# Optimization experiments

Measured on AMD Instinct MI355X. Metric: run time of the kernel, lower is better.

The kernel has to match this reference:

```python
import jax, jax.numpy as jnp
import numpy as np

DMODEL = 512
NUM_HEADS = 8
HEAD_DIM = DMODEL // NUM_HEADS
ATTN_LEN = 5
BATCH = 4
SEQ = 4096


def kv_roll(t, layer, shift):
    # t: [B, h_sub, T, 1, hd]; replicates tf.pad + tf.roll + concat + slice
    T = t.shape[2]
    dil = 2 ** layer
    p = dil * (ATTN_LEN // 2)
    tp = jnp.pad(t, ((0, 0), (0, 0), (p, p), (0, 0), (0, 0)))
    # circular rolls, concat along the singleton window axis -> [B,h,T+2p,ATTN_LEN,hd]
    rolled = jnp.concatenate(
        [jnp.roll(tp, -i * dil, axis=2) for i in range(shift, ATTN_LEN + shift)],
        axis=3,
    )
    return rolled[:, :, :T]


def setup_inputs() -> dict:
    key = jax.random.key(0)
    ks = jax.random.split(key, 8)
    inputs = jax.random.normal(ks[0], (BATCH, SEQ, DMODEL), dtype=jnp.float32)
    Wq = jax.random.normal(ks[1], (DMODEL, DMODEL), dtype=jnp.float32) * 0.02
    bq = jnp.zeros((DMODEL,), dtype=jnp.float32)
    Wk = jax.random.normal(ks[2], (DMODEL, DMODEL), dtype=jnp.float32) * 0.02
    bk = jnp.zeros((DMODEL,), dtype=jnp.float32)
    Wv = jax.random.normal(ks[3], (DMODEL, DMODEL), dtype=jnp.float32) * 0.02
    bv = jnp.zeros((DMODEL,), dtype=jnp.float32)
    Er = jax.random.normal(ks[4], (NUM_HEADS, HEAD_DIM, ATTN_LEN), dtype=jnp.float32) * 0.05
    return {"inputs": inputs, "Wq": Wq, "bq": bq, "Wk": Wk, "bk": bk,
            "Wv": Wv, "bv": bv, "Er": Er, "layer": 1}


def reference(inputs, Wq, bq, Wk, bk, Wv, bv, Er, layer):
    B, T, D = inputs.shape
    # projections -> [B, H, T, 1, hd]
    def proj(W, b):
        x = inputs @ W + b
        x = x.reshape(B, T, NUM_HEADS, 1, HEAD_DIM)
        return jnp.transpose(x, (0, 2, 1, 3, 4))
    q = proj(Wq, bq)
    k = proj(Wk, bk)
    v = proj(Wv, bv)

    def build_windows(t):
        # per-head-group shifts: heads 0-3 shift 0, head 4 shift -2, head 5 -1, head 6 +1, head 7 +2
        return jnp.concatenate((
            kv_roll(t[:, 0:4], layer, 0),
            kv_roll(t[:, 4:5], layer, -2),
            kv_roll(t[:, 5:6], layer, -1),
            kv_roll(t[:, 6:7], layer, 1),
            kv_roll(t[:, 7:8], layer, 2),
        ), axis=1)  # [B, H, T, ATTN_LEN, hd]

    kw = build_windows(k)
    vw = build_windows(v)

    # qk: [B, H, T, 1, ATTN_LEN]
    qk = jnp.einsum('bhtqd,bhtwd->bhtqw', q, kw)
    # relative positional bias: q @ Er -> [B, H, T, 1, ATTN_LEN]
    qEr = jnp.einsum('bhtqd,hdw->bhtqw', q, Er)
    scale = jnp.sqrt(jnp.float32(HEAD_DIM)).astype(inputs.dtype)
    logits = (qk + qEr) / scale
    mask = (qk == 0).astype(logits.dtype)
    attn = jax.nn.softmax(logits + mask * -10000.0, axis=-1)
    # out: [B, H, T, 1, hd]
    out = jnp.einsum('bhtqw,bhtwd->bhtqd', attn, vw)
    out = jnp.transpose(out[:, :, :, 0, :], (0, 2, 1, 3)).reshape(B, T, D)
    return out, attn
```

## Files before the change

### kernel.cpp

```cpp
#include <hip/hip_runtime.h>
#include <stdint.h>

#define B_ 4
#define T_ 4096
#define D_ 512
#define H_ 8
#define HD_ 64
#define W_ 5
#define M_ (B_*T_)
#define TILE 128
#define HALO 16
#define TMg 160
#define TN 192
#define LSTR 72

#define STEP_ 11264
#define BOFF_ 5120
#define SH_ELEMS 32256

typedef __attribute__((ext_vector_type(8))) short short8;
typedef __attribute__((ext_vector_type(4))) float floatx4;

__device__ __forceinline__ unsigned short f2bf(float f) {
    unsigned int u = __builtin_bit_cast(unsigned int, f);
    u += 0x7fffu + ((u >> 16) & 1u);
    return (unsigned short)(u >> 16);
}
__device__ __forceinline__ float bf2f(unsigned short s) {
    unsigned int u = ((unsigned int)s) << 16;
    return __builtin_bit_cast(float, u);
}
__device__ __forceinline__ void load8bf(const unsigned short* p, float* f) {
    uint4 d = *(const uint4*)p;
    f[0] = bf2f((unsigned short)(d.x & 0xffffu));
    f[1] = bf2f((unsigned short)(d.x >> 16));
    f[2] = bf2f((unsigned short)(d.y & 0xffffu));
    f[3] = bf2f((unsigned short)(d.y >> 16));
    f[4] = bf2f((unsigned short)(d.z & 0xffffu));
    f[5] = bf2f((unsigned short)(d.z >> 16));
    f[6] = bf2f((unsigned short)(d.w & 0xffffu));
    f[7] = bf2f((unsigned short)(d.w >> 16));
}

__device__ __forceinline__ void async16(const unsigned short* g, unsigned short* l) {
    __builtin_amdgcn_global_load_lds(
        (const __attribute__((address_space(1))) unsigned int*)g,
        (__attribute__((address_space(3))) unsigned int*)l, 16, 0, 0);
}

__global__ __launch_bounds__(256) void prep(const float* __restrict__ x,
                                            const float* __restrict__ Wq,
                                            const float* __restrict__ Wk,
                                            const float* __restrict__ Wv,
                                            unsigned short* __restrict__ xb,
                                            unsigned short* __restrict__ Wt2) {
    int bx = blockIdx.x;
    if (bx < 4096) {
        int i = bx * 256 + threadIdx.x;
        const float4* x4 = (const float4*)x;
        float4 a = x4[2*i], b = x4[2*i + 1];
        uint4 o;
        o.x = (unsigned)f2bf(a.x) | ((unsigned)f2bf(a.y) << 16);
        o.y = (unsigned)f2bf(a.z) | ((unsigned)f2bf(a.w) << 16);
        o.z = (unsigned)f2bf(b.x) | ((unsigned)f2bf(b.y) << 16);
        o.w = (unsigned)f2bf(b.z) | ((unsigned)f2bf(b.w) << 16);
        ((uint4*)xb)[i] = o;
    } else {
        int tid = (bx - 4096) * 256 + threadIdx.x;
        int np = tid % 1536;
        int kc = tid / 1536;
        int h = np / 192, n192 = np % 192;
        int sel = n192 >> 6, ch = n192 & 63;
        int c = h * 64 + ch;
        const float* Wsrc = (sel == 0) ? Wq : ((sel == 1) ? Wk : Wv);
        unsigned short us[8];
#pragma unroll
        for (int j = 0; j < 8; j++)
            us[j] = f2bf(Wsrc[(size_t)(kc*8 + j) * D_ + c]);
        uint4 o;
        o.x = (unsigned)us[0] | ((unsigned)us[1] << 16);
        o.y = (unsigned)us[2] | ((unsigned)us[3] << 16);
        o.z = (unsigned)us[4] | ((unsigned)us[5] << 16);
        o.w = (unsigned)us[6] | ((unsigned)us[7] << 16);
        *(uint4*)(Wt2 + (size_t)np * D_ + kc*8) = o;
    }
}

__global__ __launch_bounds__(512, 4) void fused_qkv_attn(
    const unsigned short* __restrict__ Xb,
    const unsigned short* __restrict__ Wt2,
    const float* __restrict__ bq, const float* __restrict__ bk2,
    const float* __restrict__ bv, const float* __restrict__ Er,
    const int* __restrict__ layer_p,
    float* __restrict__ out,
    float* __restrict__ attn_out)
{
    __shared__ unsigned short SH[SH_ELEMS];
    __shared__ float sEr[HD_ * W_];
    unsigned short* Qs = SH;
    unsigned short* Ks = SH + TILE * LSTR;
    unsigned short* Vs = SH + (TILE + TMg) * LSTR;

    const int tid = threadIdx.x;
    const int wave = tid >> 6, lane = tid & 63;
    const int tile = blockIdx.x >> 3, h = blockIdx.x & 7;
    const int b = tile >> 5;
    const int t0 = (tile & 31) * TILE;
    const long m0g = (long)b * T_ + t0;

    float erv = 0.f;
    if (tid < HD_ * W_) erv = Er[h * HD_ * W_ + tid];

    const unsigned short* gsrc[3] = {Xb, Xb, Xb};
    int ldoff[3] = {0, 0, 0};
#pragma unroll
    for (int j = 0; j < 3; j++) {
        int q = wave + j * 8;
        if (q < 22) {
            if (q < 10) {
                long grow = m0g - HALO + q*16 + (lane >> 2);
                grow = grow < 0 ? 0 : (grow >= M_ ? M_ - 1 : grow);
                gsrc[j] = Xb + grow * D_ + (lane & 3) * 8;
                ldoff[j] = q * 512;
            } else {
                int q2 = q - 10;
                gsrc[j] = Wt2 + ((size_t)h*TN + q2*16 + (lane >> 2)) * D_ + (lane & 3) * 8;
                ldoff[j] = BOFF_ + q2 * 512;
            }
        }
    }

    auto issue = [&](int ss) {
        unsigned short* bb = SH + (ss & 1) * STEP_;
#pragma unroll
        for (int j = 0; j < 3; j++)
            if (wave + j * 8 < 22)
                async16(gsrc[j] + ss * 32, bb + ldoff[j]);
    };

    const int wm = (wave >> 2) * 80;
    const int wn = (wave & 3) * 48;
    const int qd = lane >> 4, r16 = lane & 15;
    floatx4 acc[5][3] = {};

    issue(0);
    __syncthreads();

    #pragma unroll
    for (int s = 0; s < 16; s++) {
        if (s < 15) issue(s + 1);

        const unsigned short* bufA = SH + (s & 1) * STEP_;
        const unsigned short* bufB = bufA + BOFF_;
        short8 af[5], bfr[3];
#pragma unroll
        for (int mi = 0; mi < 5; mi++)
            af[mi] = __builtin_bit_cast(short8,
                *(const uint4*)(bufA + (wm + mi*16 + r16)*32 + qd*8));
#pragma unroll
        for (int ni = 0; ni < 3; ni++)
            bfr[ni] = __builtin_bit_cast(short8,
                *(const uint4*)(bufB + (wn + ni*16 + r16)*32 + qd*8));

        __builtin_amdgcn_s_setprio(1);
#pragma unroll
        for (int mi = 0; mi < 5; mi++)
#pragma unroll
            for (int ni = 0; ni < 3; ni++)
                acc[mi][ni] = __builtin_amdgcn_mfma_f32_16x16x32_bf16(
                    af[mi], bfr[ni], acc[mi][ni], 0, 0, 0);
        __builtin_amdgcn_s_setprio(0);

        __syncthreads();
    }

#pragma unroll
    for (int ni = 0; ni < 3; ni++) {
        int n192 = wn + ni * 16 + r16;
        int sel = n192 >> 6;
        int ch = n192 & 63;
        float bias = (sel == 0) ? bq[h*64 + ch]
                   : (sel == 1) ? bk2[h*64 + ch] : bv[h*64 + ch];
#pragma unroll
        for (int mi = 0; mi < 5; mi++)
#pragma unroll
            for (int r = 0; r < 4; r++) {
                int l = wm + mi*16 + qd*4 + r;
                unsigned short vb = f2bf(acc[mi][ni][r] + bias);
                if (sel == 0) {
                    if (l >= HALO && l < HALO + TILE)
                        Qs[(l - HALO) * LSTR + ch] = vb;
                } else if (sel == 1) {
                    Ks[l * LSTR + ch] = vb;
                } else {
                    Vs[l * LSTR + ch] = vb;
                }
            }
    }
    if (tid < HD_ * W_) sEr[tid] = erv;
    __syncthreads();

    const int dil = 1 << layer_p[0];
    const int sh = (h < 4) ? 0 : (h == 4 ? -2 : (h == 5 ? -1 : (h == 6 ? 1 : 2)));
    const int c8 = tid & 7, g64 = tid >> 3;

#pragma unroll
    for (int p = 0; p < 2; p++) {
        int tl = g64 + p * 64;
        int t = t0 + tl;
        float qf[8]; load8bf(Qs + tl * LSTR + c8 * 8, qf);

        int pos[W_]; bool val[W_]; float s[W_];
#pragma unroll
        for (int w = 0; w < W_; w++) {
            pos[w] = t + (sh + w - 2) * dil;
            val[w] = (pos[w] >= 0) && (pos[w] < T_);
            float a = 0.f;
            if (val[w]) {
                float kf[8]; load8bf(Ks + (pos[w] - t0 + HALO) * LSTR + c8 * 8, kf);
#pragma unroll
                for (int j = 0; j < 8; j++) a = fmaf(qf[j], kf[j], a);
            }
#pragma unroll
            for (int j = 0; j < 8; j++)
                a = fmaf(qf[j], sEr[(c8*8 + j) * W_ + w], a);
            s[w] = a;
        }
#pragma unroll
        for (int off = 4; off > 0; off >>= 1)
#pragma unroll
            for (int w = 0; w < W_; w++)
                s[w] += __shfl_xor(s[w], off, 8);

        float logit[W_], mx = -1e30f;
#pragma unroll
        for (int w = 0; w < W_; w++) {
            logit[w] = val[w] ? s[w] * 0.125f : -1e30f;
            mx = fmaxf(mx, logit[w]);
        }
        float pw[W_], ssum = 0.f;
#pragma unroll
        for (int w = 0; w < W_; w++) {
            pw[w] = val[w] ? __expf(logit[w] - mx) : 0.f;
            ssum += pw[w];
        }
        const float inv = 1.f / ssum;
        float aw[W_];
#pragma unroll
        for (int w = 0; w < W_; w++) aw[w] = pw[w] * inv;

        if (c8 < W_)
            attn_out[((size_t)(b * H_ + h) * T_ + t) * W_ + c8] = aw[c8];

        float of[8] = {0,0,0,0,0,0,0,0};
#pragma unroll
        for (int w = 0; w < W_; w++) {
            if (val[w]) {
                float vf[8]; load8bf(Vs + (pos[w] - t0 + HALO) * LSTR + c8 * 8, vf);
#pragma unroll
                for (int j = 0; j < 8; j++) of[j] = fmaf(aw[w], vf[j], of[j]);
            }
        }
        float* orow = out + ((size_t)b * T_ + t) * D_ + h * HD_ + c8 * 8;
        *(float4*)(orow)     = make_float4(of[0], of[1], of[2], of[3]);
        *(float4*)(orow + 4) = make_float4(of[4], of[5], of[6], of[7]);
    }
}

extern "C" void kernel_launch(void* const* d_in, const int* in_sizes, int n_in,
                              void* d_out, int out_size, void* d_ws, size_t ws_size,
                              hipStream_t stream) {
    const float* x   = (const float*)d_in[0];
    const float* Wq  = (const float*)d_in[1];
    const float* bq  = (const float*)d_in[2];
    const float* Wk  = (const float*)d_in[3];
    const float* bk  = (const float*)d_in[4];
    const float* Wv  = (const float*)d_in[5];
    const float* bv  = (const float*)d_in[6];
    const float* Er  = (const float*)d_in[7];
    const int* layer = (const int*)d_in[8];

    char* ws = (char*)d_ws;
    unsigned short* Xb  = (unsigned short*)ws;
    unsigned short* Wt2 = (unsigned short*)(ws + (size_t)16*1024*1024);

    float* out  = (float*)d_out;
    float* attn = out + (size_t)B_ * T_ * D_;

    prep<<<4096 + 384, 256, 0, stream>>>(x, Wq, Wk, Wv, Xb, Wt2);
    fused_qkv_attn<<<(M_ / TILE) * 8, 512, 0, stream>>>(Xb, Wt2, bq, bk, bv,
                                                        Er, layer, out, attn);
}
```

Before: 155.4 us.

## Shrink halo and LDS footprint with XOR swizzle to raise occupancy

Cuts the halo from 16 to 8 rows, so the GEMM M-extent drops from 160 to 144 and the lower wave group computes 4 row-tiles instead of 5. The padded LDS stride of 72 becomes an unpadded 64-wide layout with an XOR swizzle to avoid bank conflicts, and the Er table is stored in bf16. Together these shrink shared memory so launch bounds can ask for 6 blocks per CU, aiming for higher occupancy and less redundant halo projection work. A halo of 8 still covers the maximum window offset of 8 at layer 1. Rounding Er to bf16 slightly lowers precision, and any larger dilation would fall outside the halo.

```diff
diff --git a/kernel.cpp b/kernel.cpp
--- a/kernel.cpp
+++ b/kernel.cpp
@@ -9,14 +9,13 @@
 #define W_ 5
 #define M_ (B_*T_)
 #define TILE 128
-#define HALO 16
-#define TMg 160
+#define HALO 8
+#define TMg 144
 #define TN 192
-#define LSTR 72
-
-#define STEP_ 11264
-#define BOFF_ 5120
-#define SH_ELEMS 32256
+
+#define STEP_ 10752
+#define BOFF_ 4608
+#define SH_ELEMS 26624
 
 typedef __attribute__((ext_vector_type(8))) short short8;
 typedef __attribute__((ext_vector_type(4))) float floatx4;
@@ -40,6 +39,13 @@
     f[5] = bf2f((unsigned short)(d.z >> 16));
     f[6] = bf2f((unsigned short)(d.w & 0xffffu));
     f[7] = bf2f((unsigned short)(d.w >> 16));
+}
+
+__device__ __forceinline__ int swz(int row, int ch) {
+    return row * 64 + ((((ch >> 3) ^ (row & 7)) << 3) | (ch & 7));
+}
+__device__ __forceinline__ int swz8(int row, int c8) {
+    return row * 64 + ((c8 ^ (row & 7)) << 3);
 }
 
 __device__ __forceinline__ void async16(const unsigned short* g, unsigned short* l) {
@@ -86,7 +92,7 @@
     }
 }
 
-__global__ __launch_bounds__(512, 4) void fused_qkv_attn(
+__global__ __launch_bounds__(512, 6) void fused_qkv_attn(
     const unsigned short* __restrict__ Xb,
     const unsigned short* __restrict__ Wt2,
     const float* __restrict__ bq, const float* __restrict__ bk2,
@@ -96,10 +102,10 @@
     float* __restrict__ attn_out)
 {
     __shared__ unsigned short SH[SH_ELEMS];
-    __shared__ float sEr[HD_ * W_];
+    __shared__ unsigned short sEr[HD_ * W_];
     unsigned short* Qs = SH;
-    unsigned short* Ks = SH + TILE * LSTR;
-    unsigned short* Vs = SH + (TILE + TMg) * LSTR;
+    unsigned short* Ks = SH + TILE * 64;
+    unsigned short* Vs = SH + (TILE + TMg) * 64;
 
     const int tid = threadIdx.x;
     const int wave = tid >> 6, lane = tid & 63;
@@ -116,14 +122,14 @@
 #pragma unroll
     for (int j = 0; j < 3; j++) {
         int q = wave + j * 8;
-        if (q < 22) {
-            if (q < 10) {
+        if (q < 21) {
+            if (q < 9) {
                 long grow = m0g - HALO + q*16 + (lane >> 2);
                 grow = grow < 0 ? 0 : (grow >= M_ ? M_ - 1 : grow);
                 gsrc[j] = Xb + grow * D_ + (lane & 3) * 8;
                 ldoff[j] = q * 512;
             } else {
-                int q2 = q - 10;
+                int q2 = q - 9;
                 gsrc[j] = Wt2 + ((size_t)h*TN + q2*16 + (lane >> 2)) * D_ + (lane & 3) * 8;
                 ldoff[j] = BOFF_ + q2 * 512;
             }
@@ -134,11 +140,13 @@
         unsigned short* bb = SH + (ss & 1) * STEP_;
 #pragma unroll
         for (int j = 0; j < 3; j++)
-            if (wave + j * 8 < 22)
+            if (wave + j * 8 < 21)
                 async16(gsrc[j] + ss * 32, bb + ldoff[j]);
     };
 
-    const int wm = (wave >> 2) * 80;
+    const int rg = wave >> 2;
+    const int wm = rg * 80;
+    const int nm = rg ? 4 : 5;
     const int wn = (wave & 3) * 48;
     const int qd = lane >> 4, r16 = lane & 15;
     floatx4 acc[5][3] = {};
@@ -155,8 +163,9 @@
         short8 af[5], bfr[3];
 #pragma unroll
         for (int mi = 0; mi < 5; mi++)
-            af[mi] = __builtin_bit_cast(short8,
-                *(const uint4*)(bufA + (wm + mi*16 + r16)*32 + qd*8));
+            if (mi < nm)
+                af[mi] = __builtin_bit_cast(short8,
+                    *(const uint4*)(bufA + (wm + mi*16 + r16)*32 + qd*8));
 #pragma unroll
         for (int ni = 0; ni < 3; ni++)
             bfr[ni] = __builtin_bit_cast(short8,
@@ -165,10 +174,11 @@
         __builtin_amdgcn_s_setprio(1);
 #pragma unroll
         for (int mi = 0; mi < 5; mi++)
-#pragma unroll
-            for (int ni = 0; ni < 3; ni++)
-                acc[mi][ni] = __builtin_amdgcn_mfma_f32_16x16x32_bf16(
-                    af[mi], bfr[ni], acc[mi][ni], 0, 0, 0);
+            if (mi < nm)
+#pragma unroll
+                for (int ni = 0; ni < 3; ni++)
+                    acc[mi][ni] = __builtin_amdgcn_mfma_f32_16x16x32_bf16(
+                        af[mi], bfr[ni], acc[mi][ni], 0, 0, 0);
         __builtin_amdgcn_s_setprio(0);
 
         __syncthreads();
@@ -183,21 +193,22 @@
                    : (sel == 1) ? bk2[h*64 + ch] : bv[h*64 + ch];
 #pragma unroll
         for (int mi = 0; mi < 5; mi++)
-#pragma unroll
-            for (int r = 0; r < 4; r++) {
-                int l = wm + mi*16 + qd*4 + r;
-                unsigned short vb = f2bf(acc[mi][ni][r] + bias);
-                if (sel == 0) {
-                    if (l >= HALO && l < HALO + TILE)
-                        Qs[(l - HALO) * LSTR + ch] = vb;
-                } else if (sel == 1) {
-                    Ks[l * LSTR + ch] = vb;
-                } else {
-                    Vs[l * LSTR + ch] = vb;
+            if (mi < nm)
+#pragma unroll
+                for (int r = 0; r < 4; r++) {
+                    int l = wm + mi*16 + qd*4 + r;
+                    unsigned short vb = f2bf(acc[mi][ni][r] + bias);
+                    if (sel == 0) {
+                        if (l >= HALO && l < HALO + TILE)
+                            Qs[swz(l - HALO, ch)] = vb;
+                    } else if (sel == 1) {
+                        Ks[swz(l, ch)] = vb;
+                    } else {
+                        Vs[swz(l, ch)] = vb;
+                    }
                 }
-            }
-    }
-    if (tid < HD_ * W_) sEr[tid] = erv;
+    }
+    if (tid < HD_ * W_) sEr[tid] = f2bf(erv);
     __syncthreads();
 
     const int dil = 1 << layer_p[0];
@@ -208,7 +219,7 @@
     for (int p = 0; p < 2; p++) {
         int tl = g64 + p * 64;
         int t = t0 + tl;
-        float qf[8]; load8bf(Qs + tl * LSTR + c8 * 8, qf);
+        float qf[8]; load8bf(Qs + swz8(tl, c8), qf);
 
         int pos[W_]; bool val[W_]; float s[W_];
 #pragma unroll
@@ -217,13 +228,13 @@
             val[w] = (pos[w] >= 0) && (pos[w] < T_);
             float a = 0.f;
             if (val[w]) {
-                float kf[8]; load8bf(Ks + (pos[w] - t0 + HALO) * LSTR + c8 * 8, kf);
+                float kf[8]; load8bf(Ks + swz8(pos[w] - t0 + HALO, c8), kf);
 #pragma unroll
                 for (int j = 0; j < 8; j++) a = fmaf(qf[j], kf[j], a);
             }
 #pragma unroll
             for (int j = 0; j < 8; j++)
-                a = fmaf(qf[j], sEr[(c8*8 + j) * W_ + w], a);
+                a = fmaf(qf[j], bf2f(sEr[(c8*8 + j) * W_ + w]), a);
             s[w] = a;
         }
 #pragma unroll
@@ -256,7 +267,7 @@
 #pragma unroll
         for (int w = 0; w < W_; w++) {
             if (val[w]) {
-                float vf[8]; load8bf(Vs + (pos[w] - t0 + HALO) * LSTR + c8 * 8, vf);
+                float vf[8]; load8bf(Vs + swz8(pos[w] - t0 + HALO, c8), vf);
 #pragma unroll
                 for (int j = 0; j < 8; j++) of[j] = fmaf(aw[w], vf[j], of[j]);
             }
```

Result: slower. 256.1 us (+64.8%).
